# Optimization experiments

Hardware: AMD Instinct MI355X
Metric: run time of the kernel (lower is better)

## Reference

```python
import jax, jax.numpy as jnp
import numpy as np

DT = 3600.0  # Euler step size (seconds)
N = 2_097_152  # number of timesteps = len(t)


def _get_AB(params):
    """Build the 3x3 A and 3x5 B RC-network matrices from the 7 parameters."""
    Cai, Cwe, Cwi, Re, Ri, Rw, Rg = (params[i] for i in range(7))
    z = jnp.zeros((), params.dtype)
    A = jnp.stack([
        jnp.stack([-1.0 / Cai * (1.0 / Rg + 1.0 / Ri), z, 1.0 / (Cai * Ri)]),
        jnp.stack([z, -1.0 / Cwe * (1.0 / Re + 1.0 / Rw), 1.0 / (Cwe * Rw)]),
        jnp.stack([1.0 / (Cwi * Ri), 1.0 / (Cwi * Rw), -1.0 / Cwi * (1.0 / Rw + 1.0 / Ri)]),
    ])  # [3,3]
    B = jnp.stack([
        jnp.stack([1.0 / (Cai * Rg), 1.0 / Cai, 1.0 / Cai, z, z]),
        jnp.stack([1.0 / (Cwe * Re), z, z, 1.0 / Cwe, z]),
        jnp.stack([z, z, z, z, 1.0 / Cwi]),
    ])  # [3,5]
    return A, B


def setup_inputs() -> dict:
    key = jax.random.key(0)
    d = jax.random.normal(key, (N, 5), dtype=jnp.float32)  # disturbance inputs per step
    params = jnp.array([100000.0, 30000.0, 300000.0, 10.0, 1.0, 10.0, 10.0], dtype=jnp.float32)
    x0 = jnp.array([20.0, 30.0, 26.0], dtype=jnp.float32)  # initial state temps
    return {"params": params, "x0": x0, "d": d}


def reference(params, x0, d):
    # One explicit-Euler step per timestep:
    #   x_{i+1} = x_i + dt*(A x_i + B d_i) = M x_i + c_i,  M = I + dt*A, c_i = dt*B d_i
    A, B = _get_AB(params)
    M = jnp.eye(3, dtype=params.dtype) + DT * A  # [3,3]
    c = DT * (d[:-1] @ B.T)  # [N-1,3]; last row of d is unused (loop runs len(t)-1 steps)

    def step(x, ci):
        xn = M @ x + ci
        return xn, xn

    _, xs = jax.lax.scan(step, x0, c)  # xs: [N-1,3]
    return jnp.concatenate([x0[None, :], xs], axis=0)  # [N,3] == x_all
```

## Files before the change

### kernel.cpp

```cpp
#include <hip/hip_runtime.h>


static constexpr int  TPB   = 256;
static constexpr int  CHUNK = 2048;
static constexpr int  NBLK  = 1024;
static constexpr long NROW  = 2097152;

#define WS_TOT 0
#define WS_TAB 3072

struct Coef {
    float m00,m02,m11,m12,m20,m21,m22;
    float b00,b01,b10,b13,b24;
};

__device__ __forceinline__ Coef derive(const float* __restrict__ p){
    Coef o;
    const float dt = 3600.0f;
    float Cai=p[0],Cwe=p[1],Cwi=p[2],Re=p[3],Ri=p[4],Rw=p[5],Rg=p[6];
    o.m00 = 1.0f + dt * (-1.0f/Cai*(1.0f/Rg + 1.0f/Ri));
    o.m02 = dt * (1.0f/(Cai*Ri));
    o.m11 = 1.0f + dt * (-1.0f/Cwe*(1.0f/Re + 1.0f/Rw));
    o.m12 = dt * (1.0f/(Cwe*Rw));
    o.m20 = dt * (1.0f/(Cwi*Ri));
    o.m21 = dt * (1.0f/(Cwi*Rw));
    o.m22 = 1.0f + dt * (-1.0f/Cwi*(1.0f/Rw + 1.0f/Ri));
    o.b00 = dt * (1.0f/(Cai*Rg));
    o.b01 = dt * (1.0f/Cai);
    o.b10 = dt * (1.0f/(Cwe*Re));
    o.b13 = dt * (1.0f/Cwe);
    o.b24 = dt * (1.0f/Cwi);
    return o;
}

__device__ __forceinline__ void step(const Coef& C, float& s0, float& s1, float& s2,
                                     float d0, float d1, float d2, float d3, float d4){
    float c0 = fmaf(C.b00, d0, C.b01*(d1+d2));
    float c1 = fmaf(C.b10, d0, C.b13*d3);
    float c2 = C.b24*d4;
    float n0 = fmaf(C.m00, s0, fmaf(C.m02, s2, c0));
    float n1 = fmaf(C.m11, s1, fmaf(C.m12, s2, c1));
    float n2 = fmaf(C.m20, s0, fmaf(C.m21, s1, fmaf(C.m22, s2, c2)));
    s0=n0; s1=n1; s2=n2;
}

__device__ __forceinline__ void mm3(const double* X, const double* Y, double* Z){
    #pragma unroll
    for (int r=0;r<3;++r)
        #pragma unroll
        for (int c=0;c<3;++c)
            Z[r*3+c] = X[r*3+0]*Y[0*3+c] + X[r*3+1]*Y[1*3+c] + X[r*3+2]*Y[2*3+c];
}
__device__ __forceinline__ void msq(double* X){ double T[9]; mm3(X,X,T);
    #pragma unroll
    for (int i=0;i<9;++i) X[i]=T[i]; }

__device__ __forceinline__ void computeM(const float* __restrict__ p, double* Md){
    double Cai=p[0],Cwe=p[1],Cwi=p[2],Re=p[3],Ri=p[4],Rw=p[5],Rg=p[6];
    const double dt = 3600.0;
    Md[0]=1.0 - dt*((1.0/Rg + 1.0/Ri)/Cai); Md[1]=0.0;                              Md[2]=dt/(Cai*Ri);
    Md[3]=0.0;                              Md[4]=1.0 - dt*((1.0/Re + 1.0/Rw)/Cwe); Md[5]=dt/(Cwe*Rw);
    Md[6]=dt/(Cwi*Ri);                      Md[7]=dt/(Cwi*Rw);                      Md[8]=1.0 - dt*((1.0/Rw + 1.0/Ri)/Cwi);
}

__global__ __launch_bounds__(256) void k_tot(const float* __restrict__ d,
                                             const float* __restrict__ p,
                                             float* __restrict__ ws){
    int t = threadIdx.x, b = blockIdx.x;
    if (b == NBLK){
        if (t == 0){
            double A[9], M0[9], T[9];
            computeM(p, M0);
            #pragma unroll
            for (int i=0;i<9;++i) A[i]=M0[i];
            for (int k=1;k<=8;++k){
                for (int i=0;i<9;++i) ws[WS_TAB + (k-1)*9 + i] = (float)A[i];
                if (k<8){ mm3(M0, A, T); for(int i=0;i<9;++i) A[i]=T[i]; }
            }
            for (int l=0;l<8;++l){
                for (int i=0;i<9;++i) ws[WS_TAB + 72 + l*9 + i] = (float)A[i];
                msq(A);
            }
            for (int i2=0;i2<10;++i2){
                for (int i=0;i<9;++i) ws[WS_TAB + 144 + i2*9 + i] = (float)A[i];
                msq(A);
            }
        }
        return;
    }

    __shared__ float sh[CHUNK*5];
    __shared__ float Pw[8][9];
    __shared__ float Gg[9];
    __shared__ float wred[4][3];

    long base = (long)b * CHUNK;
    const float4* gsrc = (const float4*)(d + base*5);
    float4* sh4 = (float4*)sh;
    float4 stg[10];
    #pragma unroll
    for (int g=0; g<10; ++g) stg[g] = gsrc[g*TPB + t];
    if (t == 0){
        double A[9]; computeM(p, A);
        for (int i2=0;i2<8;++i2){
            for (int i=0;i<9;++i) Pw[i2][i] = (float)A[i];
            msq(A);
        }
        for (int i=0;i<9;++i) Gg[i] = (float)A[i];
    }
    #pragma unroll
    for (int g=0; g<10; ++g) sh4[g*TPB + t] = stg[g];
    __syncthreads();

    Coef C = derive(p);
    float v0,v1,v2;
    {
        const float* r = &sh[t*5];
        v0 = fmaf(C.b00, r[0], C.b01*(r[1]+r[2]));
        v1 = fmaf(C.b10, r[0], C.b13*r[3]);
        v2 = C.b24*r[4];
    }
    #pragma unroll
    for (int j=1;j<8;++j){
        const float* r = &sh[(j*TPB + t)*5];
        float c0 = fmaf(C.b00, r[0], C.b01*(r[1]+r[2]));
        float c1 = fmaf(C.b10, r[0], C.b13*r[3]);
        float c2 = C.b24*r[4];
        float n0 = Gg[0]*v0+Gg[1]*v1+Gg[2]*v2 + c0;
        float n1 = Gg[3]*v0+Gg[4]*v1+Gg[5]*v2 + c1;
        float n2 = Gg[6]*v0+Gg[7]*v1+Gg[8]*v2 + c2;
        v0=n0;v1=n1;v2=n2;
    }
    int e = 255 - t;
    #pragma unroll
    for (int i2=0;i2<8;++i2){
        float m0 = Pw[i2][0]*v0+Pw[i2][1]*v1+Pw[i2][2]*v2;
        float m1 = Pw[i2][3]*v0+Pw[i2][4]*v1+Pw[i2][5]*v2;
        float m2 = Pw[i2][6]*v0+Pw[i2][7]*v1+Pw[i2][8]*v2;
        bool bit = (e>>i2)&1;
        v0 = bit?m0:v0; v1 = bit?m1:v1; v2 = bit?m2:v2;
    }
    #pragma unroll
    for (int m=1;m<64;m<<=1){
        v0 += __shfl_xor(v0, m, 64);
        v1 += __shfl_xor(v1, m, 64);
        v2 += __shfl_xor(v2, m, 64);
    }
    int wv = t>>6, ln = t&63;
    if (ln==0){ wred[wv][0]=v0; wred[wv][1]=v1; wred[wv][2]=v2; }
    __syncthreads();
    if (t==0){
        ws[WS_TOT + b*3+0] = wred[0][0]+wred[1][0]+wred[2][0]+wred[3][0];
        ws[WS_TOT + b*3+1] = wred[0][1]+wred[1][1]+wred[2][1]+wred[3][1];
        ws[WS_TOT + b*3+2] = wred[0][2]+wred[1][2]+wred[2][2]+wred[3][2];
    }
}

__global__ __launch_bounds__(256) void k_scan(const float* __restrict__ d,
                                              const float* __restrict__ p,
                                              const float* __restrict__ ws,
                                              const float* __restrict__ x0,
                                              float* __restrict__ out){
    __shared__ float BUF[CHUNK*5];
    __shared__ float tab[234];
    __shared__ float wred[4][3];
    __shared__ float carryL[3];

    int t = threadIdx.x, b = blockIdx.x;
    long base = (long)b * CHUNK;
    const float4* gsrc = (const float4*)(d + base*5);
    float4* sh4 = (float4*)BUF;
    float4 stg[10];
    #pragma unroll
    for (int g=0; g<10; ++g) stg[g] = gsrc[g*TPB + t];
    if (t < 234) tab[t] = ws[WS_TAB + t];
    #pragma unroll
    for (int g=0; g<10; ++g) sh4[g*TPB + t] = stg[g];
    __syncthreads();

    Coef C = derive(p);
    float px[8][3];
    {
        float s0=0.f, s1=0.f, s2=0.f;
        #pragma unroll
        for (int j=0;j<8;++j){
            const float* r = &BUF[(8*t + j)*5];
            step(C, s0,s1,s2, r[0],r[1],r[2],r[3],r[4]);
            px[j][0]=s0; px[j][1]=s1; px[j][2]=s2;
        }
    }

    float w0=0.f, w1=0.f, w2=0.f;
    if (t < b){
        int e = b-1-t;
        int m = e>>8, u = e&255;
        const float* G2 = &tab[144 + 8*9];
        float a0 = ws[WS_TOT + t*3+0], a1 = ws[WS_TOT + t*3+1], a2 = ws[WS_TOT + t*3+2];
        for (int j=1;j<=m;++j){
            int kk = 256*j + t;
            float n0 = G2[0]*a0+G2[1]*a1+G2[2]*a2 + ws[WS_TOT+kk*3+0];
            float n1 = G2[3]*a0+G2[4]*a1+G2[5]*a2 + ws[WS_TOT+kk*3+1];
            float n2 = G2[6]*a0+G2[7]*a1+G2[8]*a2 + ws[WS_TOT+kk*3+2];
            a0=n0;a1=n1;a2=n2;
        }
        #pragma unroll
        for (int i2=0;i2<8;++i2){
            const float* P = &tab[144 + i2*9];
            float m0 = P[0]*a0+P[1]*a1+P[2]*a2;
            float m1 = P[3]*a0+P[4]*a1+P[5]*a2;
            float m2 = P[6]*a0+P[7]*a1+P[8]*a2;
            bool bit = (u>>i2)&1;
            a0 = bit?m0:a0; a1=bit?m1:a1; a2=bit?m2:a2;
        }
        w0=a0; w1=a1; w2=a2;
    }
    if (t == 0){
        float a0=x0[0], a1=x0[1], a2=x0[2];
        #pragma unroll
        for (int i2=0;i2<10;++i2){
            const float* P = &tab[144 + i2*9];
            float m0 = P[0]*a0+P[1]*a1+P[2]*a2;
            float m1 = P[3]*a0+P[4]*a1+P[5]*a2;
            float m2 = P[6]*a0+P[7]*a1+P[8]*a2;
            bool bit = (b>>i2)&1;
            a0 = bit?m0:a0; a1=bit?m1:a1; a2=bit?m2:a2;
        }
        w0+=a0; w1+=a1; w2+=a2;
    }
    #pragma unroll
    for (int m2v=1;m2v<64;m2v<<=1){
        w0 += __shfl_xor(w0, m2v, 64);
        w1 += __shfl_xor(w1, m2v, 64);
        w2 += __shfl_xor(w2, m2v, 64);
    }
    int wv=t>>6, ln=t&63;
    if (ln==0){ wred[wv][0]=w0; wred[wv][1]=w1; wred[wv][2]=w2; }
    __syncthreads();
    if (t==0){
        carryL[0]=wred[0][0]+wred[1][0]+wred[2][0]+wred[3][0];
        carryL[1]=wred[0][1]+wred[1][1]+wred[2][1]+wred[3][1];
        carryL[2]=wred[0][2]+wred[1][2]+wred[2][2]+wred[3][2];
    }
    __syncthreads();
    float c0=carryL[0], c1=carryL[1], c2=carryL[2];

    float* Sl = &BUF[8192];
    float z0=px[7][0], z1=px[7][1], z2=px[7][2];
    if (t==0){
        const float* M8 = &tab[72];
        z0 += M8[0]*c0+M8[1]*c1+M8[2]*c2;
        z1 += M8[3]*c0+M8[4]*c1+M8[5]*c2;
        z2 += M8[6]*c0+M8[7]*c1+M8[8]*c2;
    }
    Sl[t*3+0]=z0; Sl[t*3+1]=z1; Sl[t*3+2]=z2;
    __syncthreads();
    #pragma unroll
    for (int l=0;l<8;++l){
        const float* P = &tab[72 + l*9];
        int off = 1<<l;
        float y0=0.f,y1=0.f,y2=0.f;
        if (t>=off){ y0=Sl[(t-off)*3+0]; y1=Sl[(t-off)*3+1]; y2=Sl[(t-off)*3+2]; }
        __syncthreads();
        if (t>=off){
            z0 += P[0]*y0+P[1]*y1+P[2]*y2;
            z1 += P[3]*y0+P[4]*y1+P[5]*y2;
            z2 += P[6]*y0+P[7]*y1+P[8]*y2;
            Sl[t*3+0]=z0; Sl[t*3+1]=z1; Sl[t*3+2]=z2;
        }
        __syncthreads();
    }
    float s0,s1,s2;
    if (t==0){ s0=c0; s1=c1; s2=c2; }
    else     { s0=Sl[(t-1)*3+0]; s1=Sl[(t-1)*3+1]; s2=Sl[(t-1)*3+2]; }

    float* ost = BUF;
    #pragma unroll
    for (int j=0;j<8;++j){
        const float* P = &tab[j*9];
        float o0 = px[j][0] + P[0]*s0+P[1]*s1+P[2]*s2;
        float o1 = px[j][1] + P[3]*s0+P[4]*s1+P[5]*s2;
        float o2 = px[j][2] + P[6]*s0+P[7]*s1+P[8]*s2;
        int q = 24*t + 3 + 3*j;
        ost[q+0]=o0; ost[q+1]=o1; ost[q+2]=o2;
    }
    __syncthreads();
    float* og = out + base*3;
    const float4* ost4 = (const float4*)ost;
    float4* og4 = (float4*)og;
    #pragma unroll
    for (int g=0; g<6; ++g){
        int f = g*TPB + t;
        if (f != 0) og4[f] = ost4[f];
    }
    if (t == 0){
        og[3] = ost[3];
        if (b == 0){ out[0]=x0[0]; out[1]=x0[1]; out[2]=x0[2]; }
        if (b != NBLK-1){ og[6144]=ost[6144]; og[6145]=ost[6145]; og[6146]=ost[6146]; }
    }
}

extern "C" void kernel_launch(void* const* d_in, const int* in_sizes, int n_in,
                              void* d_out, int out_size, void* d_ws, size_t ws_size,
                              hipStream_t stream) {
    const float* params = (const float*)d_in[0];
    const float* x0     = (const float*)d_in[1];
    const float* d      = (const float*)d_in[2];
    float* out = (float*)d_out;
    float* ws  = (float*)d_ws;

    k_tot <<<NBLK+1, TPB, 0, stream>>>(d, params, ws);
    k_scan<<<NBLK,   TPB, 0, stream>>>(d, params, ws, x0, out);
}
```

Baseline: 48.85 us.

## Fuse two-pass scan into single-pass kernel with decoupled lookback via atomic slots

Replaces the reduce-then-scan pair of kernels with a tiny init kernel plus one scan kernel. Each block takes a dynamic index from an atomic ticket, computes its local chunk aggregate, and publishes it to a flag-guarded global slot. Blocks then spin-wait on their predecessors' slots to build the carry. This removes the second full read of the input, and per-thread inputs are now read straight into registers instead of staged through shared memory. The cost is spin-wait latency along the dependency chain and strided, less coalesced global loads.

```diff
diff --git a/kernel.cpp b/kernel.cpp
--- a/kernel.cpp
+++ b/kernel.cpp
@@ -4,10 +4,10 @@
 static constexpr int  TPB   = 256;
 static constexpr int  CHUNK = 2048;
 static constexpr int  NBLK  = 1024;
-static constexpr long NROW  = 2097152;
-
-#define WS_TOT 0
-#define WS_TAB 3072
+
+#define WS_SLOT 0
+#define WS_TAB  4096
+#define WS_TICK 4352
 
 struct Coef {
     float m00,m02,m11,m12,m20,m21,m22;
@@ -63,195 +63,84 @@
     Md[6]=dt/(Cwi*Ri);                      Md[7]=dt/(Cwi*Rw);                      Md[8]=1.0 - dt*((1.0/Rw + 1.0/Ri)/Cwi);
 }
 
-__global__ __launch_bounds__(256) void k_tot(const float* __restrict__ d,
-                                             const float* __restrict__ p,
-                                             float* __restrict__ ws){
-    int t = threadIdx.x, b = blockIdx.x;
-    if (b == NBLK){
-        if (t == 0){
-            double A[9], M0[9], T[9];
-            computeM(p, M0);
-            #pragma unroll
-            for (int i=0;i<9;++i) A[i]=M0[i];
-            for (int k=1;k<=8;++k){
-                for (int i=0;i<9;++i) ws[WS_TAB + (k-1)*9 + i] = (float)A[i];
-                if (k<8){ mm3(M0, A, T); for(int i=0;i<9;++i) A[i]=T[i]; }
-            }
-            for (int l=0;l<8;++l){
-                for (int i=0;i<9;++i) ws[WS_TAB + 72 + l*9 + i] = (float)A[i];
-                msq(A);
-            }
-            for (int i2=0;i2<10;++i2){
-                for (int i=0;i<9;++i) ws[WS_TAB + 144 + i2*9 + i] = (float)A[i];
-                msq(A);
-            }
-        }
-        return;
-    }
-
-    __shared__ float sh[CHUNK*5];
-    __shared__ float Pw[8][9];
-    __shared__ float Gg[9];
-    __shared__ float wred[4][3];
-
+__device__ __forceinline__ void read_slot(unsigned int* slots, int k,
+                                          float& a0, float& a1, float& a2){
+    while (__hip_atomic_load(&slots[k*4+3], __ATOMIC_ACQUIRE, __HIP_MEMORY_SCOPE_AGENT) == 0u) {}
+    a0 = __uint_as_float(__hip_atomic_load(&slots[k*4+0], __ATOMIC_RELAXED, __HIP_MEMORY_SCOPE_AGENT));
+    a1 = __uint_as_float(__hip_atomic_load(&slots[k*4+1], __ATOMIC_RELAXED, __HIP_MEMORY_SCOPE_AGENT));
+    a2 = __uint_as_float(__hip_atomic_load(&slots[k*4+2], __ATOMIC_RELAXED, __HIP_MEMORY_SCOPE_AGENT));
+}
+
+__global__ __launch_bounds__(1024) void k_init(const float* __restrict__ p,
+                                               float* __restrict__ ws){
+    int t = threadIdx.x;
+    unsigned int* w = (unsigned int*)ws;
+    w[WS_SLOT + t*4+0]=0u; w[WS_SLOT + t*4+1]=0u; w[WS_SLOT + t*4+2]=0u; w[WS_SLOT + t*4+3]=0u;
+    if (t==0){
+        w[WS_TICK] = 0u;
+        double A[9], M0[9], T[9];
+        computeM(p, M0);
+        #pragma unroll
+        for (int i=0;i<9;++i) A[i]=M0[i];
+        for (int k=1;k<=8;++k){
+            for (int i=0;i<9;++i) ws[WS_TAB + (k-1)*9 + i] = (float)A[i];
+            if (k<8){ mm3(M0, A, T); for(int i=0;i<9;++i) A[i]=T[i]; }
+        }
+        for (int l=0;l<8;++l){
+            for (int i=0;i<9;++i) ws[WS_TAB + 72 + l*9 + i] = (float)A[i];
+            msq(A);
+        }
+        for (int i2=0;i2<10;++i2){
+            for (int i=0;i<9;++i) ws[WS_TAB + 144 + i2*9 + i] = (float)A[i];
+            msq(A);
+        }
+    }
+}
+
+__global__ __launch_bounds__(256, 4) void k_one(const float* __restrict__ d,
+                                                const float* __restrict__ p,
+                                                float* __restrict__ ws,
+                                                const float* __restrict__ x0,
+                                                float* __restrict__ out){
+    __shared__ float SH[7172];
+    __shared__ int Bsh;
+    float* tab    = SH;
+    float* wred   = SH + 236;
+    float* carryL = SH + 248;
+    float* Sl     = SH + 256;
+    float* ost    = SH + 1024;
+
+    unsigned int* slots = (unsigned int*)ws + WS_SLOT;
+    unsigned int* tick  = (unsigned int*)ws + WS_TICK;
+    const float*  wsTab = ws + WS_TAB;
+
+    int t = threadIdx.x;
+    if (t==0) Bsh = (int)atomicAdd(tick, 1u);
+    if (t<234) tab[t] = wsTab[t];
+    __syncthreads();
+    int b = Bsh;
     long base = (long)b * CHUNK;
-    const float4* gsrc = (const float4*)(d + base*5);
-    float4* sh4 = (float4*)sh;
-    float4 stg[10];
-    #pragma unroll
-    for (int g=0; g<10; ++g) stg[g] = gsrc[g*TPB + t];
-    if (t == 0){
-        double A[9]; computeM(p, A);
-        for (int i2=0;i2<8;++i2){
-            for (int i=0;i<9;++i) Pw[i2][i] = (float)A[i];
-            msq(A);
-        }
-        for (int i=0;i<9;++i) Gg[i] = (float)A[i];
-    }
-    #pragma unroll
-    for (int g=0; g<10; ++g) sh4[g*TPB + t] = stg[g];
-    __syncthreads();
+
+    const float4* dp = (const float4*)(d + (base + 8L*t)*5);
+    float4 q[10];
+    #pragma unroll
+    for (int g=0; g<10; ++g) q[g] = dp[g];
 
     Coef C = derive(p);
-    float v0,v1,v2;
-    {
-        const float* r = &sh[t*5];
-        v0 = fmaf(C.b00, r[0], C.b01*(r[1]+r[2]));
-        v1 = fmaf(C.b10, r[0], C.b13*r[3]);
-        v2 = C.b24*r[4];
-    }
-    #pragma unroll
-    for (int j=1;j<8;++j){
-        const float* r = &sh[(j*TPB + t)*5];
-        float c0 = fmaf(C.b00, r[0], C.b01*(r[1]+r[2]));
-        float c1 = fmaf(C.b10, r[0], C.b13*r[3]);
-        float c2 = C.b24*r[4];
-        float n0 = Gg[0]*v0+Gg[1]*v1+Gg[2]*v2 + c0;
-        float n1 = Gg[3]*v0+Gg[4]*v1+Gg[5]*v2 + c1;
-        float n2 = Gg[6]*v0+Gg[7]*v1+Gg[8]*v2 + c2;
-        v0=n0;v1=n1;v2=n2;
-    }
-    int e = 255 - t;
-    #pragma unroll
-    for (int i2=0;i2<8;++i2){
-        float m0 = Pw[i2][0]*v0+Pw[i2][1]*v1+Pw[i2][2]*v2;
-        float m1 = Pw[i2][3]*v0+Pw[i2][4]*v1+Pw[i2][5]*v2;
-        float m2 = Pw[i2][6]*v0+Pw[i2][7]*v1+Pw[i2][8]*v2;
-        bool bit = (e>>i2)&1;
-        v0 = bit?m0:v0; v1 = bit?m1:v1; v2 = bit?m2:v2;
-    }
-    #pragma unroll
-    for (int m=1;m<64;m<<=1){
-        v0 += __shfl_xor(v0, m, 64);
-        v1 += __shfl_xor(v1, m, 64);
-        v2 += __shfl_xor(v2, m, 64);
-    }
-    int wv = t>>6, ln = t&63;
-    if (ln==0){ wred[wv][0]=v0; wred[wv][1]=v1; wred[wv][2]=v2; }
-    __syncthreads();
-    if (t==0){
-        ws[WS_TOT + b*3+0] = wred[0][0]+wred[1][0]+wred[2][0]+wred[3][0];
-        ws[WS_TOT + b*3+1] = wred[0][1]+wred[1][1]+wred[2][1]+wred[3][1];
-        ws[WS_TOT + b*3+2] = wred[0][2]+wred[1][2]+wred[2][2]+wred[3][2];
-    }
-}
-
-__global__ __launch_bounds__(256) void k_scan(const float* __restrict__ d,
-                                              const float* __restrict__ p,
-                                              const float* __restrict__ ws,
-                                              const float* __restrict__ x0,
-                                              float* __restrict__ out){
-    __shared__ float BUF[CHUNK*5];
-    __shared__ float tab[234];
-    __shared__ float wred[4][3];
-    __shared__ float carryL[3];
-
-    int t = threadIdx.x, b = blockIdx.x;
-    long base = (long)b * CHUNK;
-    const float4* gsrc = (const float4*)(d + base*5);
-    float4* sh4 = (float4*)BUF;
-    float4 stg[10];
-    #pragma unroll
-    for (int g=0; g<10; ++g) stg[g] = gsrc[g*TPB + t];
-    if (t < 234) tab[t] = ws[WS_TAB + t];
-    #pragma unroll
-    for (int g=0; g<10; ++g) sh4[g*TPB + t] = stg[g];
-    __syncthreads();
-
-    Coef C = derive(p);
+    float r[40];
+    #pragma unroll
+    for (int g=0; g<10; ++g){ r[4*g]=q[g].x; r[4*g+1]=q[g].y; r[4*g+2]=q[g].z; r[4*g+3]=q[g].w; }
     float px[8][3];
     {
         float s0=0.f, s1=0.f, s2=0.f;
         #pragma unroll
         for (int j=0;j<8;++j){
-            const float* r = &BUF[(8*t + j)*5];
-            step(C, s0,s1,s2, r[0],r[1],r[2],r[3],r[4]);
+            step(C, s0,s1,s2, r[5*j],r[5*j+1],r[5*j+2],r[5*j+3],r[5*j+4]);
             px[j][0]=s0; px[j][1]=s1; px[j][2]=s2;
         }
     }
 
-    float w0=0.f, w1=0.f, w2=0.f;
-    if (t < b){
-        int e = b-1-t;
-        int m = e>>8, u = e&255;
-        const float* G2 = &tab[144 + 8*9];
-        float a0 = ws[WS_TOT + t*3+0], a1 = ws[WS_TOT + t*3+1], a2 = ws[WS_TOT + t*3+2];
-        for (int j=1;j<=m;++j){
-            int kk = 256*j + t;
-            float n0 = G2[0]*a0+G2[1]*a1+G2[2]*a2 + ws[WS_TOT+kk*3+0];
-            float n1 = G2[3]*a0+G2[4]*a1+G2[5]*a2 + ws[WS_TOT+kk*3+1];
-            float n2 = G2[6]*a0+G2[7]*a1+G2[8]*a2 + ws[WS_TOT+kk*3+2];
-            a0=n0;a1=n1;a2=n2;
-        }
-        #pragma unroll
-        for (int i2=0;i2<8;++i2){
-            const float* P = &tab[144 + i2*9];
-            float m0 = P[0]*a0+P[1]*a1+P[2]*a2;
-            float m1 = P[3]*a0+P[4]*a1+P[5]*a2;
-            float m2 = P[6]*a0+P[7]*a1+P[8]*a2;
-            bool bit = (u>>i2)&1;
-            a0 = bit?m0:a0; a1=bit?m1:a1; a2=bit?m2:a2;
-        }
-        w0=a0; w1=a1; w2=a2;
-    }
-    if (t == 0){
-        float a0=x0[0], a1=x0[1], a2=x0[2];
-        #pragma unroll
-        for (int i2=0;i2<10;++i2){
-            const float* P = &tab[144 + i2*9];
-            float m0 = P[0]*a0+P[1]*a1+P[2]*a2;
-            float m1 = P[3]*a0+P[4]*a1+P[5]*a2;
-            float m2 = P[6]*a0+P[7]*a1+P[8]*a2;
-            bool bit = (b>>i2)&1;
-            a0 = bit?m0:a0; a1=bit?m1:a1; a2=bit?m2:a2;
-        }
-        w0+=a0; w1+=a1; w2+=a2;
-    }
-    #pragma unroll
-    for (int m2v=1;m2v<64;m2v<<=1){
-        w0 += __shfl_xor(w0, m2v, 64);
-        w1 += __shfl_xor(w1, m2v, 64);
-        w2 += __shfl_xor(w2, m2v, 64);
-    }
-    int wv=t>>6, ln=t&63;
-    if (ln==0){ wred[wv][0]=w0; wred[wv][1]=w1; wred[wv][2]=w2; }
-    __syncthreads();
-    if (t==0){
-        carryL[0]=wred[0][0]+wred[1][0]+wred[2][0]+wred[3][0];
-        carryL[1]=wred[0][1]+wred[1][1]+wred[2][1]+wred[3][1];
-        carryL[2]=wred[0][2]+wred[1][2]+wred[2][2]+wred[3][2];
-    }
-    __syncthreads();
-    float c0=carryL[0], c1=carryL[1], c2=carryL[2];
-
-    float* Sl = &BUF[8192];
     float z0=px[7][0], z1=px[7][1], z2=px[7][2];
-    if (t==0){
-        const float* M8 = &tab[72];
-        z0 += M8[0]*c0+M8[1]*c1+M8[2]*c2;
-        z1 += M8[3]*c0+M8[4]*c1+M8[5]*c2;
-        z2 += M8[6]*c0+M8[7]*c1+M8[8]*c2;
-    }
     Sl[t*3+0]=z0; Sl[t*3+1]=z1; Sl[t*3+2]=z2;
     __syncthreads();
     #pragma unroll
@@ -269,19 +158,91 @@
         }
         __syncthreads();
     }
-    float s0,s1,s2;
-    if (t==0){ s0=c0; s1=c1; s2=c2; }
-    else     { s0=Sl[(t-1)*3+0]; s1=Sl[(t-1)*3+1]; s2=Sl[(t-1)*3+2]; }
-
-    float* ost = BUF;
+    float e0=0.f,e1=0.f,e2=0.f;
+    if (t>0){ e0=Sl[(t-1)*3+0]; e1=Sl[(t-1)*3+1]; e2=Sl[(t-1)*3+2]; }
+
+    if (t==TPB-1){
+        __hip_atomic_store(&slots[b*4+0], __float_as_uint(z0), __ATOMIC_RELAXED, __HIP_MEMORY_SCOPE_AGENT);
+        __hip_atomic_store(&slots[b*4+1], __float_as_uint(z1), __ATOMIC_RELAXED, __HIP_MEMORY_SCOPE_AGENT);
+        __hip_atomic_store(&slots[b*4+2], __float_as_uint(z2), __ATOMIC_RELAXED, __HIP_MEMORY_SCOPE_AGENT);
+        __hip_atomic_store(&slots[b*4+3], 1u, __ATOMIC_RELEASE, __HIP_MEMORY_SCOPE_AGENT);
+    }
+
+    float w0=0.f, w1=0.f, w2=0.f;
+    if (t < b){
+        int e = b-1-t;
+        int m = e>>8, u = e&255;
+        const float* G2 = &tab[144 + 8*9];
+        float a0,a1,a2; read_slot(slots, t, a0,a1,a2);
+        for (int j=1;j<=m;++j){
+            int kk = 256*j + t;
+            float y0,y1,y2; read_slot(slots, kk, y0,y1,y2);
+            float n0 = G2[0]*a0+G2[1]*a1+G2[2]*a2 + y0;
+            float n1 = G2[3]*a0+G2[4]*a1+G2[5]*a2 + y1;
+            float n2 = G2[6]*a0+G2[7]*a1+G2[8]*a2 + y2;
+            a0=n0;a1=n1;a2=n2;
+        }
+        #pragma unroll
+        for (int i2=0;i2<8;++i2){
+            const float* P = &tab[144 + i2*9];
+            float m0 = P[0]*a0+P[1]*a1+P[2]*a2;
+            float m1 = P[3]*a0+P[4]*a1+P[5]*a2;
+            float m2 = P[6]*a0+P[7]*a1+P[8]*a2;
+            bool bit = (u>>i2)&1;
+            a0 = bit?m0:a0; a1=bit?m1:a1; a2=bit?m2:a2;
+        }
+        w0=a0; w1=a1; w2=a2;
+    }
+    if (t == 0){
+        float a0=x0[0], a1=x0[1], a2=x0[2];
+        #pragma unroll
+        for (int i2=0;i2<10;++i2){
+            const float* P = &tab[144 + i2*9];
+            float m0 = P[0]*a0+P[1]*a1+P[2]*a2;
+            float m1 = P[3]*a0+P[4]*a1+P[5]*a2;
+            float m2 = P[6]*a0+P[7]*a1+P[8]*a2;
+            bool bit = (b>>i2)&1;
+            a0 = bit?m0:a0; a1=bit?m1:a1; a2=bit?m2:a2;
+        }
+        w0+=a0; w1+=a1; w2+=a2;
+    }
+    #pragma unroll
+    for (int mv=1;mv<64;mv<<=1){
+        w0 += __shfl_xor(w0, mv, 64);
+        w1 += __shfl_xor(w1, mv, 64);
+        w2 += __shfl_xor(w2, mv, 64);
+    }
+    int wv=t>>6, ln=t&63;
+    if (ln==0){ wred[wv*3+0]=w0; wred[wv*3+1]=w1; wred[wv*3+2]=w2; }
+    __syncthreads();
+    if (t==0){
+        carryL[0]=wred[0]+wred[3]+wred[6]+wred[9];
+        carryL[1]=wred[1]+wred[4]+wred[7]+wred[10];
+        carryL[2]=wred[2]+wred[5]+wred[8]+wred[11];
+    }
+    __syncthreads();
+    float c0=carryL[0], c1=carryL[1], c2=carryL[2];
+
+    float a0=c0, a1=c1, a2=c2;
+    #pragma unroll
+    for (int i2=0;i2<8;++i2){
+        const float* P = &tab[72 + i2*9];
+        float m0 = P[0]*a0+P[1]*a1+P[2]*a2;
+        float m1 = P[3]*a0+P[4]*a1+P[5]*a2;
+        float m2 = P[6]*a0+P[7]*a1+P[8]*a2;
+        bool bit = (t>>i2)&1;
+        a0 = bit?m0:a0; a1=bit?m1:a1; a2=bit?m2:a2;
+    }
+    float s0=e0+a0, s1=e1+a1, s2=e2+a2;
+
     #pragma unroll
     for (int j=0;j<8;++j){
         const float* P = &tab[j*9];
         float o0 = px[j][0] + P[0]*s0+P[1]*s1+P[2]*s2;
         float o1 = px[j][1] + P[3]*s0+P[4]*s1+P[5]*s2;
         float o2 = px[j][2] + P[6]*s0+P[7]*s1+P[8]*s2;
-        int q = 24*t + 3 + 3*j;
-        ost[q+0]=o0; ost[q+1]=o1; ost[q+2]=o2;
+        int qq = 24*t + 3 + 3*j;
+        ost[qq+0]=o0; ost[qq+1]=o1; ost[qq+2]=o2;
     }
     __syncthreads();
     float* og = out + base*3;
@@ -308,6 +269,6 @@
     float* out = (float*)d_out;
     float* ws  = (float*)d_ws;
 
-    k_tot <<<NBLK+1, TPB, 0, stream>>>(d, params, ws);
-    k_scan<<<NBLK,   TPB, 0, stream>>>(d, params, ws, x0, out);
-}
+    k_init<<<1, 1024, 0, stream>>>(params, ws);
+    k_one <<<NBLK, TPB, 0, stream>>>(d, params, ws, x0, out);
+}
```

New measurement: 171.4 us. 3.51x slower.
